# Optimization experiments

Measured on AMD Instinct MI355X. Metric: run time of the kernel, lower is better.

Reference implementation:

```python
import jax, jax.numpy as jnp
import numpy as np

B, N, E, H = 2, 256, 768, 12
D = E // H
LOG_2PI = float(np.log(2.0 * np.pi))


def setup_inputs() -> dict:
    key = jax.random.key(0)
    ks = jax.random.split(key, 8)
    return {
        "x": jax.random.normal(ks[0], (B, N, E), jnp.float32),
        "Wqkv": jax.random.normal(ks[1], (E, 3 * E), jnp.float32) * 0.02,
        "bqkv": jax.random.normal(ks[2], (3 * E,), jnp.float32) * 0.02,
        "Wproj": jax.random.normal(ks[3], (E, E), jnp.float32) * 0.02,
        "bproj": jax.random.normal(ks[4], (E,), jnp.float32) * 0.02,
        "mean": jax.random.normal(ks[5], (E, E), jnp.float32),
        "logvar": jax.random.normal(ks[6], (E, E), jnp.float32),
        "mix_coef": jax.random.normal(ks[7], (E,), jnp.float32),
    }


def reference(x, Wqkv, bqkv, Wproj, bproj, mean, logvar, mix_coef):
    b, n, e = x.shape
    # qkv projection; einops 'b n (h d qkv) -> qkv b h n d' (qkv is the INNERMOST split)
    qkv = (x @ Wqkv + bqkv).reshape(b, n, H, D, 3)
    qkv = jnp.transpose(qkv, (4, 0, 2, 1, 3))  # (3, b, h, n, d)
    q, k, v = qkv[0], qkv[1], qkv[2]

    # keys back to (b, n, e): 'b h n d -> b n (h d)'
    keys = jnp.transpose(k, (0, 2, 1, 3)).reshape(b, n, e)

    # MixtureSameFamily.log_prob: component Normal batch (E, E), mixture over last dim.
    # out[b,n,i] = logsumexp_j( log_softmax(mix_coef)[j] + logN(keys[b,n,i]; mean[i,j], std[i,j]) )
    log_mix = jax.nn.log_softmax(mix_coef)                      # (E,)
    std = jnp.exp(0.5 * logvar)                                  # (E, E)
    z = (keys[:, :, :, None] - mean[None, None, :, :]) / std     # (b, n, E, E)
    comp_lp = -0.5 * (z * z) - jnp.log(std) - 0.5 * LOG_2PI      # (b, n, E, E)
    key_mix = jax.nn.logsumexp(comp_lp + log_mix, axis=-1)       # (b, n, E)

    # 'b n (h d) -> b h n d'
    key_mix = jnp.transpose(key_mix.reshape(b, n, H, D), (0, 2, 1, 3))

    energy = jnp.einsum("bhqd,bhkd->bhqk", q, key_mix)
    att = jax.nn.softmax(energy, axis=-1) / jnp.sqrt(jnp.float32(e))
    out = jnp.einsum("bhql,bhld->bhqd", att, v)                  # (b, h, n, d)
    out = jnp.transpose(out, (0, 2, 1, 3)).reshape(b, n, e)
    return out @ Wproj + bproj
```

## Files before the change

kernel.cpp:

```cpp
#include <hip/hip_runtime.h>

#define LOG2E 1.4426950408889634f
#define LN2 0.6931471805599453f

typedef __attribute__((ext_vector_type(8))) short bf16x8;
typedef __attribute__((ext_vector_type(4))) float f32x4;

constexpr int Ee = 768;
constexpr int BN = 512;
constexpr long QC_OFF = 0;
constexpr long KT_OFF = 393216;
constexpr long VC_OFF = 786432;
constexpr long P_OFF  = 1179648;
constexpr long PSTRIDE = 1179648;
constexpr long KM_OFF = 1179648;
constexpr long EN_OFF = 1572864;
constexpr long PVP_OFF = 0;
constexpr long PJP_OFF = 1179648;
constexpr long PART = 393216;

__device__ __forceinline__ unsigned pk_hi(float x0, float x1) {
    return (__float_as_uint(x0) >> 16) | (__float_as_uint(x1) & 0xFFFF0000u);
}
__device__ __forceinline__ float rhi(float x) {
    return __uint_as_float(__float_as_uint(x) & 0xFFFF0000u);
}

template<int AR>
__global__ __launch_bounds__(256)
void mfma_gemm(const float* __restrict__ A, int lda, long sAb, long sAh, long sAp,
               const float* __restrict__ Bm, int ldb, long sBb, long sBh,
               float* __restrict__ C, int ldc, long sCb, long sCh, long sCp,
               int K, int Hdiv, int KS)
{
    __shared__ __align__(16) unsigned short sm[4 * 64 * 64];
    char* const smb = (char*)sm;
    const int tid = threadIdx.x;
    const int m0 = blockIdx.x * 64, n0 = blockIdx.y * 64;
    const int kp = blockIdx.z % KS;
    const int zz = blockIdx.z / KS;
    const int zb = zz / Hdiv, zh = zz - zb * Hdiv;
    A  += zb * sAb + zh * sAh + (long)kp * K;
    Bm += zb * sBb + zh * sBh + (long)kp * (long)K * ldb;
    C  += zb * sCb + zh * sCh + (long)kp * sCp;

    const int lane = tid & 63, w = tid >> 6;
    const int wr = w >> 1, wc = w & 1;
    const int fr = lane & 15, fko2 = (lane >> 4) * 16;

    const bool isB = tid < 128;
    const int kq = isB ? (tid >> 4) : ((tid - 128) & 7);
    const int nq = tid & 15;
    const int mq = (tid - 128) >> 3;

    auto foff = [](int plane, int row, int cb) {
        return plane * 8192 + row * 128 + (cb ^ ((row & 7) << 4));
    };
    int wo[8];
    if (isB) {
        #pragma unroll
        for (int e = 0; e < 4; ++e) {
            wo[e]     = foff(2, nq * 4 + e, kq * 8);
            wo[e + 4] = foff(3, nq * 4 + e, kq * 8);
        }
    } else {
        #pragma unroll
        for (int r = 0; r < 4; ++r) {
            wo[r]     = foff(0, mq * 4 + r, kq * 8);
            wo[r + 4] = foff(1, mq * 4 + r, kq * 8);
        }
    }
    const int oA0h = foff(0, wr * 32 + fr,      fko2);
    const int oA1h = foff(0, wr * 32 + 16 + fr, fko2);
    const int oA0l = oA0h + 8192, oA1l = oA1h + 8192;
    const int oB0h = foff(2, wc * 32 + fr,      fko2);
    const int oB1h = foff(2, wc * 32 + 16 + fr, fko2);
    const int oB0l = oB0h + 8192, oB1l = oB1h + 8192;

    f32x4 acc00 = {}, acc01 = {}, acc10 = {}, acc11 = {};
    float4 r0, r1, r2, r3;

    auto load_regs = [&](int k0) {
        if (isB) {
            const float* p = &Bm[(long)(k0 + kq * 4) * ldb + n0 + nq * 4];
            r0 = *(const float4*)p; p += ldb;
            r1 = *(const float4*)p; p += ldb;
            r2 = *(const float4*)p; p += ldb;
            r3 = *(const float4*)p;
        } else {
            const float* p = &A[(long)(m0 + mq * 4) * lda + k0 + kq * 4];
            r0 = *(const float4*)p;
            if (AR == 2) { float4 t = *(const float4*)(p + sAp);
                r0.x += t.x; r0.y += t.y; r0.z += t.z; r0.w += t.w; }
            p += lda;
            r1 = *(const float4*)p;
            if (AR == 2) { float4 t = *(const float4*)(p + sAp);
                r1.x += t.x; r1.y += t.y; r1.z += t.z; r1.w += t.w; }
            p += lda;
            r2 = *(const float4*)p;
            if (AR == 2) { float4 t = *(const float4*)(p + sAp);
                r2.x += t.x; r2.y += t.y; r2.z += t.z; r2.w += t.w; }
            p += lda;
            r3 = *(const float4*)p;
            if (AR == 2) { float4 t = *(const float4*)(p + sAp);
                r3.x += t.x; r3.y += t.y; r3.z += t.z; r3.w += t.w; }
        }
    };

    auto cvt_store = [&](const float4& v, int o_hi, int o_lo) {
        uint2 hi; hi.x = pk_hi(v.x, v.y); hi.y = pk_hi(v.z, v.w);
        const float l0 = v.x - rhi(v.x), l1 = v.y - rhi(v.y);
        const float l2 = v.z - rhi(v.z), l3 = v.w - rhi(v.w);
        uint2 lo; lo.x = pk_hi(l0, l1); lo.y = pk_hi(l2, l3);
        *(uint2*)(smb + o_hi) = hi;
        *(uint2*)(smb + o_lo) = lo;
    };

    auto stage = [&]() {
        if (isB) {
            #pragma unroll
            for (int e = 0; e < 4; ++e) {
                float4 col;
                col.x = (&r0.x)[e]; col.y = (&r1.x)[e];
                col.z = (&r2.x)[e]; col.w = (&r3.x)[e];
                cvt_store(col, wo[e], wo[e + 4]);
            }
        } else {
            cvt_store(r0, wo[0], wo[4]);
            cvt_store(r1, wo[1], wo[5]);
            cvt_store(r2, wo[2], wo[6]);
            cvt_store(r3, wo[3], wo[7]);
        }
    };

    load_regs(0);
    for (int k0 = 0; k0 < K; k0 += 32) {
        __syncthreads();
        stage();
        __syncthreads();
        if (k0 + 32 < K) load_regs(k0 + 32);
        const bf16x8 Ah0 = *(const bf16x8*)(smb + oA0h);
        const bf16x8 Ah1 = *(const bf16x8*)(smb + oA1h);
        const bf16x8 Al0 = *(const bf16x8*)(smb + oA0l);
        const bf16x8 Al1 = *(const bf16x8*)(smb + oA1l);
        const bf16x8 Bh0 = *(const bf16x8*)(smb + oB0h);
        const bf16x8 Bh1 = *(const bf16x8*)(smb + oB1h);
        const bf16x8 Bl0 = *(const bf16x8*)(smb + oB0l);
        const bf16x8 Bl1 = *(const bf16x8*)(smb + oB1l);
        acc00 = __builtin_amdgcn_mfma_f32_16x16x32_bf16(Ah0, Bh0, acc00, 0, 0, 0);
        acc01 = __builtin_amdgcn_mfma_f32_16x16x32_bf16(Ah0, Bh1, acc01, 0, 0, 0);
        acc10 = __builtin_amdgcn_mfma_f32_16x16x32_bf16(Ah1, Bh0, acc10, 0, 0, 0);
        acc11 = __builtin_amdgcn_mfma_f32_16x16x32_bf16(Ah1, Bh1, acc11, 0, 0, 0);
        acc00 = __builtin_amdgcn_mfma_f32_16x16x32_bf16(Ah0, Bl0, acc00, 0, 0, 0);
        acc01 = __builtin_amdgcn_mfma_f32_16x16x32_bf16(Ah0, Bl1, acc01, 0, 0, 0);
        acc10 = __builtin_amdgcn_mfma_f32_16x16x32_bf16(Ah1, Bl0, acc10, 0, 0, 0);
        acc11 = __builtin_amdgcn_mfma_f32_16x16x32_bf16(Ah1, Bl1, acc11, 0, 0, 0);
        acc00 = __builtin_amdgcn_mfma_f32_16x16x32_bf16(Al0, Bh0, acc00, 0, 0, 0);
        acc01 = __builtin_amdgcn_mfma_f32_16x16x32_bf16(Al0, Bh1, acc01, 0, 0, 0);
        acc10 = __builtin_amdgcn_mfma_f32_16x16x32_bf16(Al1, Bh0, acc10, 0, 0, 0);
        acc11 = __builtin_amdgcn_mfma_f32_16x16x32_bf16(Al1, Bh1, acc11, 0, 0, 0);
    }

    const int rb = m0 + wr * 32 + (lane >> 4) * 4;
    const int cb = n0 + wc * 32 + fr;
    #pragma unroll
    for (int j = 0; j < 4; ++j) C[(long)(rb + j +  0) * ldc + cb +  0] = acc00[j];
    #pragma unroll
    for (int j = 0; j < 4; ++j) C[(long)(rb + j +  0) * ldc + cb + 16] = acc01[j];
    #pragma unroll
    for (int j = 0; j < 4; ++j) C[(long)(rb + j + 16) * ldc + cb +  0] = acc10[j];
    #pragma unroll
    for (int j = 0; j < 4; ++j) C[(long)(rb + j + 16) * ldc + cb + 16] = acc11[j];
}

__global__ __launch_bounds__(256)
void k_qkvreduce(const float* __restrict__ P, const float* __restrict__ bias,
                 float* __restrict__ q, float* __restrict__ kT,
                 float* __restrict__ v)
{
    const int t = blockIdx.x * 256 + threadIdx.x;
    const int row = t / 576;
    const int c4 = (t - row * 576) * 4;
    const float4 p0 = *(const float4*)&P[(long)row * 2304 + c4];
    const float4 p1 = *(const float4*)&P[PSTRIDE + (long)row * 2304 + c4];
    const float4 bb = *(const float4*)&bias[c4];
    const float r[4] = {p0.x + p1.x + bb.x, p0.y + p1.y + bb.y,
                        p0.z + p1.z + bb.z, p0.w + p1.w + bb.w};
    #pragma unroll
    for (int e = 0; e < 4; ++e) {
        const int col = c4 + e;
        const int i = col / 3, s = col - i * 3;
        if (s == 0)      q [(long)row * Ee + i]  = r[e];
        else if (s == 1) kT[(long)i * BN + row]  = r[e];
        else             v [(long)row * Ee + i]  = r[e];
    }
}

__global__ __launch_bounds__(512)
void k_mixture(const float* __restrict__ mean, const float* __restrict__ logvar,
               const float* __restrict__ mix, const float* __restrict__ keysT,
               float* __restrict__ kmT)
{
    __shared__ __align__(16) float aS[768], bS[768], cS[768];
    __shared__ float sP[512][9];
    const int i = blockIdx.x;
    const int tid = threadIdx.x;

    for (int j = tid; j < 768; j += 512) {
        const float lv = logvar[i * Ee + j];
        const float mu = mean[i * Ee + j];
        const float istd2 = __builtin_amdgcn_exp2f(-lv * LOG2E);
        aS[j] = -0.5f * LOG2E * istd2;
        bS[j] = LOG2E * mu * istd2;
        cS[j] = fmaf(-0.5f * LOG2E * mu * mu, istd2, LOG2E * (mix[j] - 0.5f * lv));
    }
    __syncthreads();

    const int rg = tid & 63;
    const int jg = tid >> 6;
    float kv[8], k2[8], s[8];
    #pragma unroll
    for (int q = 0; q < 8; ++q) {
        kv[q] = keysT[(long)i * BN + q * 64 + rg];
        k2[q] = kv[q] * kv[q];
        s[q] = 0.f;
    }
    const float4* a4 = (const float4*)(aS + jg * 96);
    const float4* b4 = (const float4*)(bS + jg * 96);
    const float4* c4 = (const float4*)(cS + jg * 96);
    for (int it = 0; it < 24; ++it) {
        const float4 a = a4[it], b = b4[it], c = c4[it];
        #pragma unroll
        for (int q = 0; q < 8; ++q) {
            s[q] += __builtin_amdgcn_exp2f(fmaf(a.x, k2[q], fmaf(b.x, kv[q], c.x)));
            s[q] += __builtin_amdgcn_exp2f(fmaf(a.y, k2[q], fmaf(b.y, kv[q], c.y)));
            s[q] += __builtin_amdgcn_exp2f(fmaf(a.z, k2[q], fmaf(b.z, kv[q], c.z)));
            s[q] += __builtin_amdgcn_exp2f(fmaf(a.w, k2[q], fmaf(b.w, kv[q], c.w)));
        }
    }
    #pragma unroll
    for (int q = 0; q < 8; ++q)
        sP[q * 64 + rg][jg] = s[q];
    __syncthreads();

    const float* rp = sP[tid];
    const float t0 = ((rp[0] + rp[1]) + (rp[2] + rp[3]))
                   + ((rp[4] + rp[5]) + (rp[6] + rp[7]));
    kmT[(long)i * BN + tid] = LN2 * __builtin_amdgcn_logf(t0);
}

__global__ __launch_bounds__(256)
void k_softmax(float* __restrict__ e)
{
    const int row = blockIdx.x * 4 + (threadIdx.x >> 6);
    const int lane = threadIdx.x & 63;
    float4* p = (float4*)(e + (long)row * 256);
    float4 v = p[lane];
    float m = fmaxf(fmaxf(v.x, v.y), fmaxf(v.z, v.w));
    #pragma unroll
    for (int off = 32; off; off >>= 1) m = fmaxf(m, __shfl_xor(m, off, 64));
    v.x = __builtin_amdgcn_exp2f((v.x - m) * LOG2E);
    v.y = __builtin_amdgcn_exp2f((v.y - m) * LOG2E);
    v.z = __builtin_amdgcn_exp2f((v.z - m) * LOG2E);
    v.w = __builtin_amdgcn_exp2f((v.w - m) * LOG2E);
    float s = v.x + v.y + v.z + v.w;
    #pragma unroll
    for (int off = 32; off; off >>= 1) s += __shfl_xor(s, off, 64);
    const float sc = 1.0f / (s * 27.712812921102035f);
    v.x *= sc; v.y *= sc; v.z *= sc; v.w *= sc;
    p[lane] = v;
}

__global__ __launch_bounds__(256)
void k_outbias(const float* __restrict__ PJ, const float* __restrict__ bias,
               float* __restrict__ out)
{
    const int t = blockIdx.x * 256 + threadIdx.x;
    const int row = t / 192;
    const int c4 = (t - row * 192) * 4;
    const float4 p0 = *(const float4*)&PJ[(long)row * 768 + c4];
    const float4 p1 = *(const float4*)&PJ[PART + (long)row * 768 + c4];
    const float4 bb = *(const float4*)&bias[c4];
    float4 v = {p0.x + p1.x + bb.x, p0.y + p1.y + bb.y,
                p0.z + p1.z + bb.z, p0.w + p1.w + bb.w};
    *(float4*)&out[(long)row * 768 + c4] = v;
}

extern "C" void kernel_launch(void* const* d_in, const int* in_sizes, int n_in,
                              void* d_out, int out_size, void* d_ws, size_t ws_size,
                              hipStream_t stream)
{
    (void)in_sizes; (void)n_in; (void)out_size; (void)ws_size;
    const float* x      = (const float*)d_in[0];
    const float* Wqkv   = (const float*)d_in[1];
    const float* bqkv   = (const float*)d_in[2];
    const float* Wproj  = (const float*)d_in[3];
    const float* bproj  = (const float*)d_in[4];
    const float* mean   = (const float*)d_in[5];
    const float* logvar = (const float*)d_in[6];
    const float* mixc   = (const float*)d_in[7];
    float* out = (float*)d_out;
    float* ws = (float*)d_ws;
    float* qc     = ws + QC_OFF;
    float* keysT  = ws + KT_OFF;
    float* vc     = ws + VC_OFF;
    float* P      = ws + P_OFF;
    float* kmT    = ws + KM_OFF;
    float* energy = ws + EN_OFF;
    float* pvp    = ws + PVP_OFF;
    float* pjp    = ws + PJP_OFF;

    mfma_gemm<1><<<dim3(8,36,2),256,0,stream>>>(
        x,768,0,0,0, Wqkv,2304,0,0, P,2304,0,0,PSTRIDE, 384, 1, 2);
    k_qkvreduce<<<1152,256,0,stream>>>(P, bqkv, qc, keysT, vc);
    k_mixture<<<768,512,0,stream>>>(mean, logvar, mixc, keysT, kmT);
    mfma_gemm<1><<<dim3(4,4,24),256,0,stream>>>(
        qc,768,196608,64,0, kmT,512,256,32768, energy,256,786432,65536,0, 64, 12, 1);
    k_softmax<<<1536,256,0,stream>>>(energy);
    mfma_gemm<1><<<dim3(4,1,48),256,0,stream>>>(
        energy,256,786432,65536,0, vc,768,196608,64, pvp,768,196608,64,PART, 128, 12, 2);
    mfma_gemm<2><<<dim3(8,12,2),256,0,stream>>>(
        pvp,768,0,0,PART, Wproj,768,0,0, pjp,768,0,0,PART, 384, 1, 2);
    k_outbias<<<384,256,0,stream>>>(pjp, bproj, out);
}
```

Before: 108.1 us.

## Drop split-K in GEMMs and fuse bias/scatter epilogues, removing reduce kernels

Removes the split-K partitioning from the QKV, PV and output projection GEMMs. The bias add and the q/k/v de-interleave scatter now run inside the GEMM epilogue, which eliminates the separate qkvreduce and outbias kernels along with their partial-sum buffers and two launches. The trade-off is half as many blocks per GEMM, so longer K loops run on a GPU with many CUs, and the scattered stores in the epilogue are uncoalesced.

```diff
diff --git a/kernel.cpp b/kernel.cpp
--- a/kernel.cpp
+++ b/kernel.cpp
@@ -11,13 +11,9 @@
 constexpr long QC_OFF = 0;
 constexpr long KT_OFF = 393216;
 constexpr long VC_OFF = 786432;
-constexpr long P_OFF  = 1179648;
-constexpr long PSTRIDE = 1179648;
 constexpr long KM_OFF = 1179648;
 constexpr long EN_OFF = 1572864;
-constexpr long PVP_OFF = 0;
-constexpr long PJP_OFF = 1179648;
-constexpr long PART = 393216;
+constexpr long OA_OFF = 3145728;
 
 __device__ __forceinline__ unsigned pk_hi(float x0, float x1) {
     return (__float_as_uint(x0) >> 16) | (__float_as_uint(x1) & 0xFFFF0000u);
@@ -26,23 +22,23 @@
     return __uint_as_float(__float_as_uint(x) & 0xFFFF0000u);
 }
 
-template<int AR>
+template<int EPI>
 __global__ __launch_bounds__(256)
-void mfma_gemm(const float* __restrict__ A, int lda, long sAb, long sAh, long sAp,
+void mfma_gemm(const float* __restrict__ A, int lda, long sAb, long sAh,
                const float* __restrict__ Bm, int ldb, long sBb, long sBh,
-               float* __restrict__ C, int ldc, long sCb, long sCh, long sCp,
-               int K, int Hdiv, int KS)
+               float* __restrict__ C, int ldc, long sCb, long sCh,
+               const float* __restrict__ bias, int K, int Hdiv,
+               float* __restrict__ eq, float* __restrict__ ek,
+               float* __restrict__ ev)
 {
     __shared__ __align__(16) unsigned short sm[4 * 64 * 64];
     char* const smb = (char*)sm;
     const int tid = threadIdx.x;
     const int m0 = blockIdx.x * 64, n0 = blockIdx.y * 64;
-    const int kp = blockIdx.z % KS;
-    const int zz = blockIdx.z / KS;
-    const int zb = zz / Hdiv, zh = zz - zb * Hdiv;
-    A  += zb * sAb + zh * sAh + (long)kp * K;
-    Bm += zb * sBb + zh * sBh + (long)kp * (long)K * ldb;
-    C  += zb * sCb + zh * sCh + (long)kp * sCp;
+    const int zb = blockIdx.z / Hdiv, zh = blockIdx.z - zb * Hdiv;
+    A  += zb * sAb + zh * sAh;
+    Bm += zb * sBb + zh * sBh;
+    C  += zb * sCb + zh * sCh;
 
     const int lane = tid & 63, w = tid >> 6;
     const int wr = w >> 1, wc = w & 1;
@@ -89,21 +85,10 @@
             r3 = *(const float4*)p;
         } else {
             const float* p = &A[(long)(m0 + mq * 4) * lda + k0 + kq * 4];
-            r0 = *(const float4*)p;
-            if (AR == 2) { float4 t = *(const float4*)(p + sAp);
-                r0.x += t.x; r0.y += t.y; r0.z += t.z; r0.w += t.w; }
-            p += lda;
-            r1 = *(const float4*)p;
-            if (AR == 2) { float4 t = *(const float4*)(p + sAp);
-                r1.x += t.x; r1.y += t.y; r1.z += t.z; r1.w += t.w; }
-            p += lda;
-            r2 = *(const float4*)p;
-            if (AR == 2) { float4 t = *(const float4*)(p + sAp);
-                r2.x += t.x; r2.y += t.y; r2.z += t.z; r2.w += t.w; }
-            p += lda;
+            r0 = *(const float4*)p; p += lda;
+            r1 = *(const float4*)p; p += lda;
+            r2 = *(const float4*)p; p += lda;
             r3 = *(const float4*)p;
-            if (AR == 2) { float4 t = *(const float4*)(p + sAp);
-                r3.x += t.x; r3.y += t.y; r3.z += t.z; r3.w += t.w; }
         }
     };
 
@@ -163,36 +148,32 @@
 
     const int rb = m0 + wr * 32 + (lane >> 4) * 4;
     const int cb = n0 + wc * 32 + fr;
-    #pragma unroll
-    for (int j = 0; j < 4; ++j) C[(long)(rb + j +  0) * ldc + cb +  0] = acc00[j];
-    #pragma unroll
-    for (int j = 0; j < 4; ++j) C[(long)(rb + j +  0) * ldc + cb + 16] = acc01[j];
-    #pragma unroll
-    for (int j = 0; j < 4; ++j) C[(long)(rb + j + 16) * ldc + cb +  0] = acc10[j];
-    #pragma unroll
-    for (int j = 0; j < 4; ++j) C[(long)(rb + j + 16) * ldc + cb + 16] = acc11[j];
-}
-
-__global__ __launch_bounds__(256)
-void k_qkvreduce(const float* __restrict__ P, const float* __restrict__ bias,
-                 float* __restrict__ q, float* __restrict__ kT,
-                 float* __restrict__ v)
-{
-    const int t = blockIdx.x * 256 + threadIdx.x;
-    const int row = t / 576;
-    const int c4 = (t - row * 576) * 4;
-    const float4 p0 = *(const float4*)&P[(long)row * 2304 + c4];
-    const float4 p1 = *(const float4*)&P[PSTRIDE + (long)row * 2304 + c4];
-    const float4 bb = *(const float4*)&bias[c4];
-    const float r[4] = {p0.x + p1.x + bb.x, p0.y + p1.y + bb.y,
-                        p0.z + p1.z + bb.z, p0.w + p1.w + bb.w};
-    #pragma unroll
-    for (int e = 0; e < 4; ++e) {
-        const int col = c4 + e;
-        const int i = col / 3, s = col - i * 3;
-        if (s == 0)      q [(long)row * Ee + i]  = r[e];
-        else if (s == 1) kT[(long)i * BN + row]  = r[e];
-        else             v [(long)row * Ee + i]  = r[e];
+    if (EPI == 1) {
+        auto scat = [&](int row, int col, float x) {
+            x += bias[col];
+            const int i = col / 3, s = col - i * 3;
+            if (s == 0)      eq[(long)row * Ee + i] = x;
+            else if (s == 1) ek[(long)i * BN + row] = x;
+            else             ev[(long)row * Ee + i] = x;
+        };
+        #pragma unroll
+        for (int j = 0; j < 4; ++j) {
+            scat(rb + j,      cb,      acc00[j]);
+            scat(rb + j,      cb + 16, acc01[j]);
+            scat(rb + j + 16, cb,      acc10[j]);
+            scat(rb + j + 16, cb + 16, acc11[j]);
+        }
+    } else {
+        const float b0  = bias ? bias[cb]      : 0.f;
+        const float b16 = bias ? bias[cb + 16] : 0.f;
+        #pragma unroll
+        for (int j = 0; j < 4; ++j) C[(long)(rb + j +  0) * ldc + cb +  0] = acc00[j] + b0;
+        #pragma unroll
+        for (int j = 0; j < 4; ++j) C[(long)(rb + j +  0) * ldc + cb + 16] = acc01[j] + b16;
+        #pragma unroll
+        for (int j = 0; j < 4; ++j) C[(long)(rb + j + 16) * ldc + cb +  0] = acc10[j] + b0;
+        #pragma unroll
+        for (int j = 0; j < 4; ++j) C[(long)(rb + j + 16) * ldc + cb + 16] = acc11[j] + b16;
     }
 }
 
@@ -269,21 +250,6 @@
     const float sc = 1.0f / (s * 27.712812921102035f);
     v.x *= sc; v.y *= sc; v.z *= sc; v.w *= sc;
     p[lane] = v;
-}
-
-__global__ __launch_bounds__(256)
-void k_outbias(const float* __restrict__ PJ, const float* __restrict__ bias,
-               float* __restrict__ out)
-{
-    const int t = blockIdx.x * 256 + threadIdx.x;
-    const int row = t / 192;
-    const int c4 = (t - row * 192) * 4;
-    const float4 p0 = *(const float4*)&PJ[(long)row * 768 + c4];
-    const float4 p1 = *(const float4*)&PJ[PART + (long)row * 768 + c4];
-    const float4 bb = *(const float4*)&bias[c4];
-    float4 v = {p0.x + p1.x + bb.x, p0.y + p1.y + bb.y,
-                p0.z + p1.z + bb.z, p0.w + p1.w + bb.w};
-    *(float4*)&out[(long)row * 768 + c4] = v;
 }
 
 extern "C" void kernel_launch(void* const* d_in, const int* in_sizes, int n_in,
@@ -304,22 +270,22 @@
     float* qc     = ws + QC_OFF;
     float* keysT  = ws + KT_OFF;
     float* vc     = ws + VC_OFF;
-    float* P      = ws + P_OFF;
     float* kmT    = ws + KM_OFF;
     float* energy = ws + EN_OFF;
-    float* pvp    = ws + PVP_OFF;
-    float* pjp    = ws + PJP_OFF;
-
-    mfma_gemm<1><<<dim3(8,36,2),256,0,stream>>>(
-        x,768,0,0,0, Wqkv,2304,0,0, P,2304,0,0,PSTRIDE, 384, 1, 2);
-    k_qkvreduce<<<1152,256,0,stream>>>(P, bqkv, qc, keysT, vc);
+    float* oat    = ws + OA_OFF;
+
+    mfma_gemm<1><<<dim3(8,36,1),256,0,stream>>>(
+        x,768,0,0, Wqkv,2304,0,0, nullptr,0,0,0, bqkv, 768, 1,
+        qc, keysT, vc);
     k_mixture<<<768,512,0,stream>>>(mean, logvar, mixc, keysT, kmT);
-    mfma_gemm<1><<<dim3(4,4,24),256,0,stream>>>(
-        qc,768,196608,64,0, kmT,512,256,32768, energy,256,786432,65536,0, 64, 12, 1);
+    mfma_gemm<0><<<dim3(4,4,24),256,0,stream>>>(
+        qc,768,196608,64, kmT,512,256,32768, energy,256,786432,65536,
+        nullptr, 64, 12, nullptr,nullptr,nullptr);
     k_softmax<<<1536,256,0,stream>>>(energy);
-    mfma_gemm<1><<<dim3(4,1,48),256,0,stream>>>(
-        energy,256,786432,65536,0, vc,768,196608,64, pvp,768,196608,64,PART, 128, 12, 2);
-    mfma_gemm<2><<<dim3(8,12,2),256,0,stream>>>(
-        pvp,768,0,0,PART, Wproj,768,0,0, pjp,768,0,0,PART, 384, 1, 2);
-    k_outbias<<<384,256,0,stream>>>(pjp, bproj, out);
-}
+    mfma_gemm<0><<<dim3(4,1,24),256,0,stream>>>(
+        energy,256,786432,65536, vc,768,196608,64, oat,768,196608,64,
+        nullptr, 256, 12, nullptr,nullptr,nullptr);
+    mfma_gemm<0><<<dim3(8,12,1),256,0,stream>>>(
+        oat,768,0,0, Wproj,768,0,0, out,768,0,0, bproj, 768, 1,
+        nullptr,nullptr,nullptr);
+}
```

Result: no change. 109.3 us (+1.1%).
